# Kernel tuning notes

Hardware: AMD Instinct MI355X
Metric: run time of the kernel (lower is better)

The kernel has to match this reference:

```python
import jax, jax.numpy as jnp
import numpy as np

B, N, C = 8, 2048, 256

def setup_inputs() -> dict:
    key = jax.random.key(0)
    ks = jax.random.split(key, 6)
    corr = jax.random.normal(ks[0], (B, N, N), dtype=jnp.float32)
    feat = jax.random.normal(ks[1], (B, N, C), dtype=jnp.float32)
    histogram = jax.random.uniform(ks[2], (B, N, 1), dtype=jnp.float32)
    mask = jax.random.normal(ks[3], (N, N), dtype=jnp.float32)
    # nn.Linear(C, C) params
    lim = 1.0 / np.sqrt(C)
    v_w = jax.random.uniform(ks[4], (C, C), minval=-lim, maxval=lim, dtype=jnp.float32)
    v_b = jax.random.uniform(ks[5], (C,), minval=-lim, maxval=lim, dtype=jnp.float32)
    return {"corr": corr, "feat": feat, "histogram": histogram, "mask": mask, "v_w": v_w, "v_b": v_b}

def reference(corr, feat, histogram, mask, v_w, v_b):
    # histogram is viewed/expanded in the original but never used downstream.
    # masked softmax over last axis: (b, n, n)
    attn = jax.nn.softmax(corr + mask[None, :, :], axis=-1)
    # v projection: y = feat @ v_w.T + v_b   (b, n, c)
    ref_feat_v = jnp.einsum("bnc,dc->bnd", feat, v_w) + v_b
    # attention output: (b, n, c)
    return jnp.einsum("bnm,bmc->bnc", attn, ref_feat_v)
```

## Files before the change

### kernel.cpp

```cpp
#include <hip/hip_runtime.h>
#include <hip/hip_fp16.h>


#define B_ 8
#define N_ 2048
#define C_ 256
#define FSZ 16384

typedef _Float16 half8  __attribute__((ext_vector_type(8)));
typedef _Float16 half4v __attribute__((ext_vector_type(4)));
typedef float    f32x4  __attribute__((ext_vector_type(4)));

static __device__ __forceinline__ void gload_lds16(const _Float16* g, _Float16* l) {
    __builtin_amdgcn_global_load_lds(
        (const __attribute__((address_space(1))) unsigned int*)g,
        (__attribute__((address_space(3))) unsigned int*)l,
        16, 0, 0);
}

__global__ __launch_bounds__(256) void k_convw(const float* __restrict__ w,
                                               _Float16* __restrict__ wh) {
    int i = (blockIdx.x * 256 + threadIdx.x) * 4;
    float4 v = *(const float4*)(w + i);
    half4v h = {(_Float16)v.x, (_Float16)v.y, (_Float16)v.z, (_Float16)v.w};
    *(half4v*)(wh + i) = h;
}

__global__ __launch_bounds__(256) void k_trans(const float* __restrict__ feat,
                                               _Float16* __restrict__ featF) {
    __shared__ _Float16 s[64][68];
    int blk  = blockIdx.x;
    int b    = blk >> 7;
    int tile = blk & 127;
    int n0   = (tile >> 2) << 6;
    int c0   = (tile & 3) << 6;
    int t    = threadIdx.x;

    const float* src = feat + ((size_t)(b * N_ + n0)) * C_ + c0;
#pragma unroll
    for (int i = 0; i < 4; ++i) {
        int idx = i * 256 + t;
        int row = idx >> 4;
        int c4  = (idx & 15) << 2;
        float4 v = *(const float4*)(src + (size_t)row * C_ + c4);
        half4v h = {(_Float16)v.x, (_Float16)v.y, (_Float16)v.z, (_Float16)v.w};
        *(half4v*)&s[row][c4] = h;
    }
    __syncthreads();

    int w = t >> 6, l = t & 63;
    int kk  = w & 1;
    int cb0 = (w >> 1) << 1;
#pragma unroll
    for (int cbi = 0; cbi < 2; ++cbi) {
        int cb = cb0 + cbi;
        half8 v;
#pragma unroll
        for (int j = 0; j < 8; ++j)
            v[j] = s[kk * 32 + ((l >> 4) << 3) + j][(cb << 4) + (l & 15)];
        _Float16* dst = featF +
            (((size_t)((b * 64 + (n0 >> 5) + kk) * 16 + (c0 >> 4) + cb)) * 64 + l) * 8;
        *(half8*)dst = v;
    }
}

__global__ __launch_bounds__(1024, 4) void k_attn(const float* __restrict__ corr,
                                                  const float* __restrict__ mask,
                                                  const _Float16* __restrict__ featF,
                                                  _Float16* __restrict__ T) {
    __shared__ _Float16 p_lds[2][64][72];
    __shared__ _Float16 f_lds[3][FSZ];
    __shared__ float rowsum[64];

    const int rblk = blockIdx.x >> 3;
    const int b    = blockIdx.x & 7;
    const int r0   = rblk * 64;
    const int tg   = threadIdx.x;
    const int w    = tg >> 6, l = tg & 63;
    const int wr   = w >> 3, wc = w & 7;
    const int lrow = l & 15, kch = l >> 4;

    const int srow = tg >> 4;
    const int scol = (tg & 15) << 2;

    const float*    pc  = corr + ((size_t)(b * N_ + r0 + srow)) * N_ + scol;
    const float*    pm  = mask + ((size_t)(r0 + srow)) * N_ + scol;
    const _Float16* pfb = featF + (size_t)b * (64 * 16 * 512);

    float rs = 0.0f;
    f32x4 acc[2][2] = {};

#define STAGE_F(TT, BUFI)                                                     \
    {                                                                         \
        _Float16* fdst = &f_lds[BUFI][0];                                     \
        const _Float16* gsrc = pfb + (size_t)(TT) * FSZ;                      \
        _Pragma("unroll")                                                     \
        for (int i_ = 0; i_ < 2; ++i_) {                                      \
            int ch_ = i_ * 16 + w;                                            \
            gload_lds16(gsrc + ch_ * 512 + l * 8, fdst + ch_ * 512);          \
        }                                                                     \
    }

#define EXPSTORE(TT, CC, MM)                                                  \
    {                                                                         \
        float p0 = __expf((CC).x + (MM).x), p1 = __expf((CC).y + (MM).y);     \
        float p2 = __expf((CC).z + (MM).z), p3 = __expf((CC).w + (MM).w);     \
        rs += (p0 + p1) + (p2 + p3);                                          \
        half4v h = {(_Float16)p0, (_Float16)p1, (_Float16)p2, (_Float16)p3};  \
        *(half4v*)&p_lds[(TT) & 1][srow][scol] = h;                           \
    }

    STAGE_F(0, 0);
    STAGE_F(1, 1);
    float4 cP = *(const float4*)pc;
    float4 mP = *(const float4*)pm;
    float4 cA = *(const float4*)(pc + 64);
    float4 mA = *(const float4*)(pm + 64);
    float4 cB, mB;
    asm volatile("s_waitcnt vmcnt(0)" ::: "memory");
    EXPSTORE(0, cP, mP);
    __syncthreads();

#define STEP(T_, CCON, MCON, CLD, MLD)                                        \
    {                                                                         \
        const int t_ = (T_);                                                  \
        if (t_ < 30) {                                                        \
            STAGE_F(t_ + 2, (t_ + 2) % 3);                                    \
            CLD = *(const float4*)(pc + (t_ + 2) * 64);                       \
            MLD = *(const float4*)(pm + (t_ + 2) * 64);                       \
        }                                                                     \
        {                                                                     \
            const _Float16* fb = &f_lds[t_ % 3][0];                           \
            const int par = t_ & 1;                                           \
            _Pragma("unroll")                                                 \
            for (int kk = 0; kk < 2; ++kk) {                                  \
                half8 a0 = *(const half8*)&p_lds[par][wr * 32 + lrow][kk * 32 + kch * 8];      \
                half8 a1 = *(const half8*)&p_lds[par][wr * 32 + 16 + lrow][kk * 32 + kch * 8]; \
                half8 b0 = *(const half8*)(fb + ((kk * 16 + wc * 2) * 64 + l) * 8);            \
                half8 b1 = *(const half8*)(fb + ((kk * 16 + wc * 2 + 1) * 64 + l) * 8);        \
                acc[0][0] = __builtin_amdgcn_mfma_f32_16x16x32_f16(a0, b0, acc[0][0], 0, 0, 0);\
                acc[0][1] = __builtin_amdgcn_mfma_f32_16x16x32_f16(a0, b1, acc[0][1], 0, 0, 0);\
                acc[1][0] = __builtin_amdgcn_mfma_f32_16x16x32_f16(a1, b0, acc[1][0], 0, 0, 0);\
                acc[1][1] = __builtin_amdgcn_mfma_f32_16x16x32_f16(a1, b1, acc[1][1], 0, 0, 0);\
            }                                                                 \
        }                                                                     \
        if (t_ < 31) EXPSTORE(t_ + 1, CCON, MCON);                            \
        if (t_ < 30) {                                                        \
            asm volatile("s_waitcnt vmcnt(4) lgkmcnt(0)" ::: "memory");       \
        } else {                                                              \
            asm volatile("s_waitcnt vmcnt(0) lgkmcnt(0)" ::: "memory");       \
        }                                                                     \
        __builtin_amdgcn_s_barrier();                                         \
    }

    for (int th = 0; th < 16; ++th) {
        STEP(2 * th,     cA, mA, cB, mB);
        STEP(2 * th + 1, cB, mB, cA, mA);
    }
#undef STEP
#undef STAGE_F
#undef EXPSTORE

    rs += __shfl_xor(rs, 1);
    rs += __shfl_xor(rs, 2);
    rs += __shfl_xor(rs, 4);
    rs += __shfl_xor(rs, 8);
    if ((l & 15) == 0) rowsum[srow] = rs;
    __syncthreads();

#pragma unroll
    for (int m = 0; m < 2; ++m) {
        float inv[4];
#pragma unroll
        for (int j = 0; j < 4; ++j)
            inv[j] = 1.0f / rowsum[wr * 32 + m * 16 + kch * 4 + j];
        _Float16* pT = T + ((size_t)(b * N_ + r0 + wr * 32 + m * 16 + kch * 4)) * C_
                         + wc * 32 + lrow;
#pragma unroll
        for (int j = 0; j < 4; ++j) {
#pragma unroll
            for (int n = 0; n < 2; ++n) {
                pT[(size_t)j * C_ + n * 16] = (_Float16)(acc[m][n][j] * inv[j]);
            }
        }
    }
}

__global__ __launch_bounds__(256, 2) void k_out(const _Float16* __restrict__ T,
                                                const _Float16* __restrict__ wh,
                                                const float* __restrict__ v_b,
                                                float* __restrict__ out) {
    const int blk = blockIdx.x;
    const int r0  = blk * 32;
    const int t   = threadIdx.x;
    const int w   = t >> 6, l = t & 63;
    const int wr  = w >> 1, wc = w & 1;
    const int lrow = l & 15, kch = l >> 4;

    const _Float16* pA = T  + ((size_t)(r0 + wr * 16 + lrow)) * C_ + kch * 8;
    const _Float16* pB = wh + ((size_t)(wc * 128 + lrow)) * C_ + kch * 8;

    f32x4 acc[8] = {};
#pragma unroll
    for (int step = 0; step < 8; step++) {
        half8 a = *(const half8*)(pA + step * 32);
#pragma unroll
        for (int q = 0; q < 8; q++) {
            half8 bf = *(const half8*)(pB + step * 32 + (size_t)q * 16 * C_);
            acc[q] = __builtin_amdgcn_mfma_f32_16x16x32_f16(a, bf, acc[q], 0, 0, 0);
        }
    }

    float* pO = out + ((size_t)(r0 + wr * 16 + kch * 4)) * C_ + wc * 128 + lrow;
#pragma unroll
    for (int q = 0; q < 8; q++) {
        float bias = v_b[wc * 128 + q * 16 + lrow];
#pragma unroll
        for (int j = 0; j < 4; j++) {
            pO[(size_t)j * C_ + q * 16] = acc[q][j] + bias;
        }
    }
}

extern "C" void kernel_launch(void* const* d_in, const int* in_sizes, int n_in,
                              void* d_out, int out_size, void* d_ws, size_t ws_size,
                              hipStream_t stream) {
    const float* corr = (const float*)d_in[0];
    const float* feat = (const float*)d_in[1];
    const float* mask = (const float*)d_in[3];
    const float* v_w  = (const float*)d_in[4];
    const float* v_b  = (const float*)d_in[5];
    float* out = (float*)d_out;

    char* ws = (char*)d_ws;
    _Float16* featF = (_Float16*)ws;
    _Float16* T     = (_Float16*)(ws + (size_t)8 * 1024 * 1024);
    _Float16* wh    = (_Float16*)(ws + (size_t)16 * 1024 * 1024);

    hipLaunchKernelGGL(k_trans, dim3(1024), dim3(256), 0, stream, feat, featF);
    hipLaunchKernelGGL(k_convw, dim3(64),   dim3(256), 0, stream, v_w, wh);
    hipLaunchKernelGGL(k_attn,  dim3(256),  dim3(1024), 0, stream, corr, mask, featF, T);
    hipLaunchKernelGGL(k_out,   dim3(512),  dim3(256), 0, stream, T, wh, v_b, out);
}
```

Measured before the change: 80.78 us.

## Shrink attention tiles to 32 rows and read feat fragments directly from global

The attention kernel now uses 512-thread blocks covering 32 rows, doubling the grid to 512 blocks. The LDS staging of feature tiles via global_load_lds is removed, and each wave reads its B fragments straight from global memory/L2. The probability tile in LDS gets an XOR swizzle to avoid bank conflicts. This cuts LDS use and barrier waits and adds parallelism, but each block re-reads all of feat for a batch, doubling global feat traffic and exposing load latency to the MFMA loop.

```diff
diff --git a/kernel.cpp b/kernel.cpp
--- a/kernel.cpp
+++ b/kernel.cpp
@@ -5,18 +5,10 @@
 #define B_ 8
 #define N_ 2048
 #define C_ 256
-#define FSZ 16384
 
 typedef _Float16 half8  __attribute__((ext_vector_type(8)));
 typedef _Float16 half4v __attribute__((ext_vector_type(4)));
 typedef float    f32x4  __attribute__((ext_vector_type(4)));
-
-static __device__ __forceinline__ void gload_lds16(const _Float16* g, _Float16* l) {
-    __builtin_amdgcn_global_load_lds(
-        (const __attribute__((address_space(1))) unsigned int*)g,
-        (__attribute__((address_space(3))) unsigned int*)l,
-        16, 0, 0);
-}
 
 __global__ __launch_bounds__(256) void k_convw(const float* __restrict__ w,
                                                _Float16* __restrict__ wh) {
@@ -64,20 +56,18 @@
     }
 }
 
-__global__ __launch_bounds__(1024, 4) void k_attn(const float* __restrict__ corr,
-                                                  const float* __restrict__ mask,
-                                                  const _Float16* __restrict__ featF,
-                                                  _Float16* __restrict__ T) {
-    __shared__ _Float16 p_lds[2][64][72];
-    __shared__ _Float16 f_lds[3][FSZ];
-    __shared__ float rowsum[64];
+__global__ __launch_bounds__(512, 4) void k_attn(const float* __restrict__ corr,
+                                                 const float* __restrict__ mask,
+                                                 const _Float16* __restrict__ featF,
+                                                 _Float16* __restrict__ T) {
+    __shared__ _Float16 p_lds[2][32 * 64];
+    __shared__ float rowsum[32];
 
     const int rblk = blockIdx.x >> 3;
     const int b    = blockIdx.x & 7;
-    const int r0   = rblk * 64;
+    const int r0   = rblk * 32;
     const int tg   = threadIdx.x;
     const int w    = tg >> 6, l = tg & 63;
-    const int wr   = w >> 3, wc = w & 7;
     const int lrow = l & 15, kch = l >> 4;
 
     const int srow = tg >> 4;
@@ -87,19 +77,12 @@
     const float*    pm  = mask + ((size_t)(r0 + srow)) * N_ + scol;
     const _Float16* pfb = featF + (size_t)b * (64 * 16 * 512);
 
+    const int swaddr = srow * 64 + (((scol >> 3) ^ (srow & 7)) << 3) + (scol & 7);
+    const int ag0 = ((kch ^ (lrow & 7)) << 3);
+    const int ag1 = (((4 + kch) ^ (lrow & 7)) << 3);
+
     float rs = 0.0f;
     f32x4 acc[2][2] = {};
-
-#define STAGE_F(TT, BUFI)                                                     \
-    {                                                                         \
-        _Float16* fdst = &f_lds[BUFI][0];                                     \
-        const _Float16* gsrc = pfb + (size_t)(TT) * FSZ;                      \
-        _Pragma("unroll")                                                     \
-        for (int i_ = 0; i_ < 2; ++i_) {                                      \
-            int ch_ = i_ * 16 + w;                                            \
-            gload_lds16(gsrc + ch_ * 512 + l * 8, fdst + ch_ * 512);          \
-        }                                                                     \
-    }
 
 #define EXPSTORE(TT, CC, MM)                                                  \
     {                                                                         \
@@ -107,17 +90,14 @@
         float p2 = __expf((CC).z + (MM).z), p3 = __expf((CC).w + (MM).w);     \
         rs += (p0 + p1) + (p2 + p3);                                          \
         half4v h = {(_Float16)p0, (_Float16)p1, (_Float16)p2, (_Float16)p3};  \
-        *(half4v*)&p_lds[(TT) & 1][srow][scol] = h;                           \
-    }
-
-    STAGE_F(0, 0);
-    STAGE_F(1, 1);
+        *(half4v*)&p_lds[(TT) & 1][swaddr] = h;                               \
+    }
+
     float4 cP = *(const float4*)pc;
     float4 mP = *(const float4*)pm;
     float4 cA = *(const float4*)(pc + 64);
     float4 mA = *(const float4*)(pm + 64);
     float4 cB, mB;
-    asm volatile("s_waitcnt vmcnt(0)" ::: "memory");
     EXPSTORE(0, cP, mP);
     __syncthreads();
 
@@ -125,32 +105,31 @@
     {                                                                         \
         const int t_ = (T_);                                                  \
         if (t_ < 30) {                                                        \
-            STAGE_F(t_ + 2, (t_ + 2) % 3);                                    \
             CLD = *(const float4*)(pc + (t_ + 2) * 64);                       \
             MLD = *(const float4*)(pm + (t_ + 2) * 64);                       \
         }                                                                     \
         {                                                                     \
-            const _Float16* fb = &f_lds[t_ % 3][0];                           \
-            const int par = t_ & 1;                                           \
+            const _Float16* pl = &p_lds[t_ & 1][0];                           \
             _Pragma("unroll")                                                 \
             for (int kk = 0; kk < 2; ++kk) {                                  \
-                half8 a0 = *(const half8*)&p_lds[par][wr * 32 + lrow][kk * 32 + kch * 8];      \
-                half8 a1 = *(const half8*)&p_lds[par][wr * 32 + 16 + lrow][kk * 32 + kch * 8]; \
-                half8 b0 = *(const half8*)(fb + ((kk * 16 + wc * 2) * 64 + l) * 8);            \
-                half8 b1 = *(const half8*)(fb + ((kk * 16 + wc * 2 + 1) * 64 + l) * 8);        \
-                acc[0][0] = __builtin_amdgcn_mfma_f32_16x16x32_f16(a0, b0, acc[0][0], 0, 0, 0);\
-                acc[0][1] = __builtin_amdgcn_mfma_f32_16x16x32_f16(a0, b1, acc[0][1], 0, 0, 0);\
-                acc[1][0] = __builtin_amdgcn_mfma_f32_16x16x32_f16(a1, b0, acc[1][0], 0, 0, 0);\
-                acc[1][1] = __builtin_amdgcn_mfma_f32_16x16x32_f16(a1, b1, acc[1][1], 0, 0, 0);\
+                const int gofs = kk ? ag1 : ag0;                              \
+                half8 a0 = *(const half8*)&pl[lrow * 64 + gofs];              \
+                half8 a1 = *(const half8*)&pl[(16 + lrow) * 64 + gofs];       \
+                const _Float16* pf =                                          \
+                    pfb + (((size_t)((2 * t_ + kk) * 16 + w * 2)) * 64 + l) * 8; \
+                half8 b0 = *(const half8*)pf;                                 \
+                half8 b1 = *(const half8*)(pf + 512);                         \
+                acc[0][0] = __builtin_amdgcn_mfma_f32_16x16x32_f16(a0, b0, acc[0][0], 0, 0, 0); \
+                acc[0][1] = __builtin_amdgcn_mfma_f32_16x16x32_f16(a0, b1, acc[0][1], 0, 0, 0); \
+                acc[1][0] = __builtin_amdgcn_mfma_f32_16x16x32_f16(a1, b0, acc[1][0], 0, 0, 0); \
+                acc[1][1] = __builtin_amdgcn_mfma_f32_16x16x32_f16(a1, b1, acc[1][1], 0, 0, 0); \
             }                                                                 \
         }                                                                     \
         if (t_ < 31) EXPSTORE(t_ + 1, CCON, MCON);                            \
-        if (t_ < 30) {                                                        \
-            asm volatile("s_waitcnt vmcnt(4) lgkmcnt(0)" ::: "memory");       \
-        } else {                                                              \
-            asm volatile("s_waitcnt vmcnt(0) lgkmcnt(0)" ::: "memory");       \
-        }                                                                     \
+        asm volatile("s_waitcnt lgkmcnt(0)" ::: "memory");                    \
+        __builtin_amdgcn_sched_barrier(0);                                    \
         __builtin_amdgcn_s_barrier();                                         \
+        __builtin_amdgcn_sched_barrier(0);                                    \
     }
 
     for (int th = 0; th < 16; ++th) {
@@ -158,7 +137,6 @@
         STEP(2 * th + 1, cB, mB, cA, mA);
     }
 #undef STEP
-#undef STAGE_F
 #undef EXPSTORE
 
     rs += __shfl_xor(rs, 1);
@@ -173,9 +151,9 @@
         float inv[4];
 #pragma unroll
         for (int j = 0; j < 4; ++j)
-            inv[j] = 1.0f / rowsum[wr * 32 + m * 16 + kch * 4 + j];
-        _Float16* pT = T + ((size_t)(b * N_ + r0 + wr * 32 + m * 16 + kch * 4)) * C_
-                         + wc * 32 + lrow;
+            inv[j] = 1.0f / rowsum[m * 16 + kch * 4 + j];
+        _Float16* pT = T + ((size_t)(b * N_ + r0 + m * 16 + kch * 4)) * C_
+                         + w * 32 + lrow;
 #pragma unroll
         for (int j = 0; j < 4; ++j) {
 #pragma unroll
@@ -239,6 +217,6 @@
 
     hipLaunchKernelGGL(k_trans, dim3(1024), dim3(256), 0, stream, feat, featF);
     hipLaunchKernelGGL(k_convw, dim3(64),   dim3(256), 0, stream, v_w, wh);
-    hipLaunchKernelGGL(k_attn,  dim3(256),  dim3(1024), 0, stream, corr, mask, featF, T);
+    hipLaunchKernelGGL(k_attn,  dim3(512),  dim3(512), 0, stream, corr, mask, featF, T);
     hipLaunchKernelGGL(k_out,   dim3(512),  dim3(256), 0, stream, T, wh, v_b, out);
 }
```

Result: faster. 76.40 us (-5.4%).
